# Optimization experiments

Hardware: AMD Instinct MI355X
Metric: run time of the kernel (lower is better)

Reference implementation:

```python
import jax, jax.numpy as jnp
import numpy as np

N = 50000          # nodes
DEG = 16           # out-degree
E = N * DEG        # edges
IN = 256           # input feature dim
H = 8              # hidden heads
DH = 32            # per-head hidden dim (hidden_dim // H)
HID = H * DH       # 256
OUT = 64           # output dim (single output head)
ALPHA = 0.2        # LeakyReLU negative slope


def _xavier(k, shape, fan_in, fan_out):
    limit = 1.414 * np.sqrt(6.0 / (fan_in + fan_out))
    return jax.random.uniform(k, shape, jnp.float32, -limit, limit)


def setup_inputs() -> dict:
    key = jax.random.key(0)
    ks = jax.random.split(key, 6)
    X = jax.random.normal(ks[0], (N, IN), jnp.float32)
    src = jnp.repeat(jnp.arange(N, dtype=jnp.int32), DEG)      # every row non-empty
    dst = jax.random.randint(ks[1], (E,), 0, N, jnp.int32)
    edges = jnp.stack([src, dst])                               # [2, E]
    W0 = _xavier(ks[2], (H, IN, DH), IN, DH)
    a0 = _xavier(ks[3], (H, 2 * DH), 2 * DH, 1)
    W1 = _xavier(ks[4], (1, HID, OUT), HID, OUT)
    a1 = _xavier(ks[5], (1, 2 * OUT), 2 * OUT, 1)
    return {"X": X, "edges": edges, "W0": W0, "a0": a0, "W1": W1, "a1": a1}


def sparse_gat_layer(X, edges, W, a):
    # W: [H, Din, D], a: [H, 2D]. Equivalent to concat(h_src, h_dst) @ a split.
    n = X.shape[0]
    D = W.shape[2]
    src, dst = edges[0], edges[1]
    h = jnp.einsum('nd,hde->hne', X, W)                         # [H, N, D]
    s_src = jnp.einsum('hne,he->hn', h, a[:, :D])               # [H, N]
    s_dst = jnp.einsum('hne,he->hn', h, a[:, D:])               # [H, N]
    e = jax.nn.leaky_relu(s_src[:, src] + s_dst[:, dst], ALPHA)  # [H, E]
    # stable per-row (segment = src) softmax, matching torch.sparse.softmax(dim=1)
    seg_max = jax.lax.stop_gradient(
        jax.vmap(lambda v: jax.ops.segment_max(v, src, num_segments=n))(e))
    p = jnp.exp(e - seg_max[:, src])
    denom = jax.vmap(lambda v: jax.ops.segment_sum(v, src, num_segments=n))(p)
    att = p / denom[:, src]                                      # [H, E]
    # out[i] = sum_{e: src=i} att_e * h[dst_e]
    agg = jax.vmap(lambda a_, hh: jax.ops.segment_sum(a_[:, None] * hh[dst], src,
                                                      num_segments=n))(att, h)
    return agg                                                   # [H, N, D]


def reference(X, edges, W0, a0, W1, a1):
    h1 = jax.nn.elu(sparse_gat_layer(X, edges, W0, a0))          # [H, N, DH]
    X1 = jnp.transpose(h1, (1, 0, 2)).reshape(X.shape[0], -1)    # concat heads [N, HID]
    out = sparse_gat_layer(X1, edges, W1, a1)                    # [1, N, OUT]
    return jax.nn.elu(out[0])                                    # num_heads_out = 1
```

## Files before the change

### kernel.cpp

```cpp
#include <hip/hip_runtime.h>

typedef __attribute__((ext_vector_type(8))) short bh8;
typedef __attribute__((ext_vector_type(4))) float f4;

static __device__ __forceinline__ float b2f(unsigned short u){
  union { unsigned int i; float f; } c; c.i = ((unsigned int)u) << 16; return c.f;
}
static __device__ __forceinline__ unsigned short f2b(float f){
  union { float f; unsigned int i; } c; c.f = f;
  unsigned int u = c.i; u += 0x7fffu + ((u >> 16) & 1u);
  return (unsigned short)(u >> 16);
}
static __device__ __forceinline__ float elu1(float x){ return x > 0.f ? x : (__expf(x) - 1.f); }
static __device__ __forceinline__ float lrelu(float x){ return x > 0.f ? x : 0.2f * x; }
static __device__ __forceinline__ float gload(const void* p, size_t i, int isf32){
  return isf32 ? ((const float*)p)[i] : b2f(((const unsigned short*)p)[i]);
}
static __device__ __forceinline__ int detect_f32(const unsigned int* __restrict__ W0w, int lane){
  unsigned int w = W0w[lane & 63];
  unsigned int e = (w >> 7) & 0xFFu;
  unsigned long long m = __ballot(e >= 100u && e <= 126u);
  return (__popcll(m) < 32) ? 1 : 0;
}

__global__ __launch_bounds__(256) void prep_kernel(
    const void* __restrict__ W0, const void* __restrict__ a0,
    const void* __restrict__ W1, const void* __restrict__ a1,
    unsigned short* __restrict__ Wt1, unsigned short* __restrict__ Wt2){
  int isf = detect_f32((const unsigned int*)W0, threadIdx.x & 63);
  int c = blockIdx.x, k = threadIdx.x;
  if (c < 272){
    float v;
    if (c < 256){
      int h = c >> 5, d = c & 31;
      v = gload(W0, (size_t)(h*256 + k)*32 + d, isf);
    } else if (c < 264){
      int h = c - 256; float s = 0.f;
      for (int d = 0; d < 32; d++)
        s += gload(W0, (size_t)(h*256 + k)*32 + d, isf) * gload(a0, h*64 + d, isf);
      v = s;
    } else {
      int h = c - 264; float s = 0.f;
      for (int d = 0; d < 32; d++)
        s += gload(W0, (size_t)(h*256 + k)*32 + d, isf) * gload(a0, h*64 + 32 + d, isf);
      v = s;
    }
    Wt1[c*256 + k] = f2b(v);
  } else {
    int c2 = c - 272; float v;
    if (c2 < 64) v = gload(W1, k*64 + c2, isf);
    else if (c2 == 64){ float s = 0.f; for (int i = 0; i < 64; i++) s += gload(W1, k*64+i, isf) * gload(a1, i, isf);      v = s; }
    else if (c2 == 65){ float s = 0.f; for (int i = 0; i < 64; i++) s += gload(W1, k*64+i, isf) * gload(a1, 64 + i, isf); v = s; }
    else v = 0.f;
    Wt2[c2*256 + k] = f2b(v);
  }
}

__global__ __launch_bounds__(256, 2) void gemm1_mfma(
    const void* __restrict__ Xraw, const unsigned short* __restrict__ Wt,
    unsigned short* __restrict__ H1, float* __restrict__ S1, int N,
    const void* __restrict__ W0){
  __shared__ __align__(16) unsigned short A[112*264];
  int tid = threadIdx.x, wv = tid >> 6, lane = tid & 63;
  int isf = detect_f32((const unsigned int*)W0, lane);
  int q = lane >> 4, l = lane & 15;
  int n0 = blockIdx.x*112;
  #pragma unroll
  for (int it = 0; it < 14; it++){
    int g = it*256 + tid;
    int r = g >> 5, c = g & 31;
    int grow = n0 + r; if (grow > N-1) grow = N-1;
    bh8 v;
    if (isf){
      const float* xr = (const float*)Xraw + (size_t)grow*256 + c*8;
      float4 u0 = *(const float4*)xr, u1 = *(const float4*)(xr + 4);
      v[0]=(short)f2b(u0.x); v[1]=(short)f2b(u0.y); v[2]=(short)f2b(u0.z); v[3]=(short)f2b(u0.w);
      v[4]=(short)f2b(u1.x); v[5]=(short)f2b(u1.y); v[6]=(short)f2b(u1.z); v[7]=(short)f2b(u1.w);
    } else {
      v = *(const bh8*)((const unsigned short*)Xraw + (size_t)grow*256 + c*8);
    }
    *(bh8*)&A[r*264 + c*8] = v;
  }
  __syncthreads();
  const bh8* Wb = (const bh8*)Wt;
  bh8 B[4][8];
  #pragma unroll
  for (int tt = 0; tt < 4; tt++){
    int t = wv*4 + tt;
    #pragma unroll
    for (int kk = 0; kk < 8; kk++) B[tt][kk] = Wb[(size_t)(t*16 + l)*32 + kk*4 + q];
  }
  bh8 Bs[8];
  if (wv == 0){
    #pragma unroll
    for (int kk = 0; kk < 8; kk++) Bs[kk] = Wb[(size_t)(256 + l)*32 + kk*4 + q];
  }
  for (int m = 0; m < 7; m++){
    bh8 a[8];
    #pragma unroll
    for (int kk = 0; kk < 8; kk++) a[kk] = *(const bh8*)&A[(m*16 + l)*264 + kk*32 + q*8];
    f4 acc[4];
    #pragma unroll
    for (int tt = 0; tt < 4; tt++){
      f4 z = {0.f,0.f,0.f,0.f}; acc[tt] = z;
      #pragma unroll
      for (int kk = 0; kk < 8; kk++)
        acc[tt] = __builtin_amdgcn_mfma_f32_16x16x32_bf16(a[kk], B[tt][kk], acc[tt], 0, 0, 0);
    }
    if (wv == 0){
      f4 as = {0.f,0.f,0.f,0.f};
      #pragma unroll
      for (int kk = 0; kk < 8; kk++)
        as = __builtin_amdgcn_mfma_f32_16x16x32_bf16(a[kk], Bs[kk], as, 0, 0, 0);
      #pragma unroll
      for (int r = 0; r < 4; r++){
        int row = n0 + m*16 + q*4 + r;
        if (row < N) S1[(size_t)row*16 + l] = as[r];
      }
    }
    __syncthreads();
    #pragma unroll
    for (int tt = 0; tt < 4; tt++){
      int t = wv*4 + tt;
      #pragma unroll
      for (int r = 0; r < 4; r++)
        A[(m*16 + q*4 + r)*264 + t*16 + l] = f2b(acc[tt][r]);
    }
    __syncthreads();
  }
  #pragma unroll
  for (int g = 0; g < 14; g++){
    int idx = g*256 + tid;
    int r = idx >> 5, c = idx & 31;
    int row = n0 + r;
    if (row < N)
      *(bh8*)(H1 + (size_t)row*256 + c*8) = *(const bh8*)&A[r*264 + c*8];
  }
}

__global__ __launch_bounds__(256) void fused_agg1_gemm2(
    const float* __restrict__ S1, const unsigned short* __restrict__ H1,
    const int* __restrict__ dst, const unsigned short* __restrict__ Wt2,
    unsigned short* __restrict__ H2, float* __restrict__ S2, int N){
  __shared__ __align__(16) unsigned short Xt[16*264];
  __shared__ __align__(16) unsigned short Hs[16*88];
  int tid = threadIdx.x, wv = tid >> 6, lane = tid & 63;
  int n0 = blockIdx.x*16;
  int h = lane >> 3, jj = lane & 7;
  int half = lane >> 5, li = lane & 31;
  int cb = li*8, hc = li >> 2;
  for (int np = 0; np < 2; np++){
    int lrA = wv*4 + np*2, lrB = lrA + 1;
    int nodeA = n0 + lrA; if (nodeA > N-1) nodeA = N-1;
    int nodeB = n0 + lrB; if (nodeB > N-1) nodeB = N-1;
    const int* dpA = dst + (size_t)nodeA*16;
    const int* dpB = dst + (size_t)nodeB*16;
    int d0A = dpA[jj], d1A = dpA[jj + 8];
    int d0B = dpB[jj], d1B = dpB[jj + 8];
    float ssA = S1[(size_t)nodeA*16 + h];
    float ssB = S1[(size_t)nodeB*16 + h];
    float e0A = lrelu(ssA + S1[(size_t)d0A*16 + 8 + h]);
    float e1A = lrelu(ssA + S1[(size_t)d1A*16 + 8 + h]);
    float e0B = lrelu(ssB + S1[(size_t)d0B*16 + 8 + h]);
    float e1B = lrelu(ssB + S1[(size_t)d1B*16 + 8 + h]);
    float mA = fmaxf(e0A, e1A), mB = fmaxf(e0B, e1B);
    mA = fmaxf(mA, __shfl_xor(mA, 1)); mB = fmaxf(mB, __shfl_xor(mB, 1));
    mA = fmaxf(mA, __shfl_xor(mA, 2)); mB = fmaxf(mB, __shfl_xor(mB, 2));
    mA = fmaxf(mA, __shfl_xor(mA, 4)); mB = fmaxf(mB, __shfl_xor(mB, 4));
    float p0A = __expf(e0A - mA), p1A = __expf(e1A - mA);
    float p0B = __expf(e0B - mB), p1B = __expf(e1B - mB);
    float sA = p0A + p1A, sB = p0B + p1B;
    sA += __shfl_xor(sA, 1); sB += __shfl_xor(sB, 1);
    sA += __shfl_xor(sA, 2); sB += __shfl_xor(sB, 2);
    sA += __shfl_xor(sA, 4); sB += __shfl_xor(sB, 4);
    float invA = 1.f / sA, invB = 1.f / sB;
    float v0A = p0A * invA, v1A = p1A * invA;
    float v0B = p0B * invB, v1B = p1B * invB;
    float accA[8] = {0.f,0.f,0.f,0.f,0.f,0.f,0.f,0.f};
    float accB[8] = {0.f,0.f,0.f,0.f,0.f,0.f,0.f,0.f};
    #pragma unroll
    for (int i = 0; i < 8; i++){
      int j  = i*2 + half;
      int jl = j & 7;
      int rowA  = (i < 4) ? __shfl(d0A, jl) : __shfl(d1A, jl);
      int rowB  = (i < 4) ? __shfl(d0B, jl) : __shfl(d1B, jl);
      float awA = (i < 4) ? __shfl(v0A, hc*8 + jl) : __shfl(v1A, hc*8 + jl);
      float awB = (i < 4) ? __shfl(v0B, hc*8 + jl) : __shfl(v1B, hc*8 + jl);
      bh8 vA = *(const bh8*)(H1 + (size_t)rowA*256 + cb);
      bh8 vB = *(const bh8*)(H1 + (size_t)rowB*256 + cb);
      #pragma unroll
      for (int c = 0; c < 8; c++){
        accA[c] += awA * b2f((unsigned short)vA[c]);
        accB[c] += awB * b2f((unsigned short)vB[c]);
      }
    }
    #pragma unroll
    for (int c = 0; c < 8; c++){
      accA[c] += __shfl_xor(accA[c], 32);
      accB[c] += __shfl_xor(accB[c], 32);
    }
    if (half == 0){
      bh8 oA, oB;
      #pragma unroll
      for (int c = 0; c < 8; c++){
        oA[c] = (short)f2b(elu1(accA[c]));
        oB[c] = (short)f2b(elu1(accB[c]));
      }
      *(bh8*)&Xt[lrA*264 + cb] = oA;
      *(bh8*)&Xt[lrB*264 + cb] = oB;
    }
  }
  __syncthreads();
  {
    int q = lane >> 4, l = lane & 15;
    bh8 a[8];
    #pragma unroll
    for (int kk = 0; kk < 8; kk++)
      a[kk] = *(const bh8*)&Xt[l*264 + kk*32 + q*8];
    const bh8* Wb = (const bh8*)Wt2;
    int ntt = (wv == 3) ? 2 : 1;
    for (int it = 0; it < ntt; it++){
      int tt = (it == 0) ? wv : 4;
      bh8 b[8];
      #pragma unroll
      for (int kk = 0; kk < 8; kk++) b[kk] = Wb[(size_t)(tt*16 + l)*32 + kk*4 + q];
      f4 c0 = {0.f,0.f,0.f,0.f};
      #pragma unroll
      for (int kk = 0; kk < 8; kk++)
        c0 = __builtin_amdgcn_mfma_f32_16x16x32_bf16(a[kk], b[kk], c0, 0, 0, 0);
      if (tt < 4){
        #pragma unroll
        for (int r = 0; r < 4; r++)
          Hs[(q*4 + r)*88 + tt*16 + l] = f2b(c0[r]);
      } else if (l < 2){
        #pragma unroll
        for (int r = 0; r < 4; r++){
          int row0 = n0 + q*4 + r;
          if (row0 < N) S2[(size_t)row0*2 + l] = c0[r];
        }
      }
    }
  }
  __syncthreads();
  if (tid < 128){
    int r2 = tid >> 3, ch = tid & 7;
    int row = n0 + r2;
    if (row < N)
      *(bh8*)(H2 + (size_t)row*64 + ch*8) = *(const bh8*)&Hs[r2*88 + ch*8];
  }
}

__global__ __launch_bounds__(256) void agg2_kernel(
    const float* __restrict__ S2, const unsigned short* __restrict__ H2,
    const int* __restrict__ dst, void* __restrict__ outv, int N,
    const void* __restrict__ W0){
  int tid = threadIdx.x, wv = tid >> 6, lane = tid & 63;
  int isf = detect_f32((const unsigned int*)W0, lane);
  int nodeA = blockIdx.x*8 + wv*2; if (nodeA > N-1) nodeA = N-1;
  int nodeB = nodeA + 1;           if (nodeB > N-1) nodeB = N-1;
  int j = lane & 15;
  int dA = dst[(size_t)nodeA*16 + j];
  int dB = dst[(size_t)nodeB*16 + j];
  float eA = lrelu(S2[(size_t)nodeA*2] + S2[(size_t)dA*2 + 1]);
  float eB = lrelu(S2[(size_t)nodeB*2] + S2[(size_t)dB*2 + 1]);
  float mA = eA, mB = eB;
  mA = fmaxf(mA, __shfl_xor(mA, 1)); mB = fmaxf(mB, __shfl_xor(mB, 1));
  mA = fmaxf(mA, __shfl_xor(mA, 2)); mB = fmaxf(mB, __shfl_xor(mB, 2));
  mA = fmaxf(mA, __shfl_xor(mA, 4)); mB = fmaxf(mB, __shfl_xor(mB, 4));
  mA = fmaxf(mA, __shfl_xor(mA, 8)); mB = fmaxf(mB, __shfl_xor(mB, 8));
  float pA = __expf(eA - mA), pB = __expf(eB - mB);
  float sA = pA, sB = pB;
  sA += __shfl_xor(sA, 1); sB += __shfl_xor(sB, 1);
  sA += __shfl_xor(sA, 2); sB += __shfl_xor(sB, 2);
  sA += __shfl_xor(sA, 4); sB += __shfl_xor(sB, 4);
  sA += __shfl_xor(sA, 8); sB += __shfl_xor(sB, 8);
  float attA = pA / sA, attB = pB / sB;
  int g = lane >> 3, cbl = (lane & 7)*8;
  float accA[8] = {0.f,0.f,0.f,0.f,0.f,0.f,0.f,0.f};
  float accB[8] = {0.f,0.f,0.f,0.f,0.f,0.f,0.f,0.f};
  #pragma unroll
  for (int it = 0; it < 2; it++){
    int j2 = it*8 + g;
    float awA = __shfl(attA, j2), awB = __shfl(attB, j2);
    int rowA  = __shfl(dA,   j2), rowB  = __shfl(dB,   j2);
    bh8 vA = *(const bh8*)(H2 + (size_t)rowA*64 + cbl);
    bh8 vB = *(const bh8*)(H2 + (size_t)rowB*64 + cbl);
    #pragma unroll
    for (int c = 0; c < 8; c++){
      accA[c] += awA * b2f((unsigned short)vA[c]);
      accB[c] += awB * b2f((unsigned short)vB[c]);
    }
  }
  #pragma unroll
  for (int c = 0; c < 8; c++){
    accA[c] += __shfl_xor(accA[c], 8);  accB[c] += __shfl_xor(accB[c], 8);
    accA[c] += __shfl_xor(accA[c], 16); accB[c] += __shfl_xor(accB[c], 16);
    accA[c] += __shfl_xor(accA[c], 32); accB[c] += __shfl_xor(accB[c], 32);
  }
  if (lane < 8){
    size_t oiA = (size_t)nodeA*64 + cbl;
    size_t oiB = (size_t)nodeB*64 + cbl;
    if (isf){
      float4 a0v, a1v, b0v, b1v;
      a0v.x = elu1(accA[0]); a0v.y = elu1(accA[1]); a0v.z = elu1(accA[2]); a0v.w = elu1(accA[3]);
      a1v.x = elu1(accA[4]); a1v.y = elu1(accA[5]); a1v.z = elu1(accA[6]); a1v.w = elu1(accA[7]);
      b0v.x = elu1(accB[0]); b0v.y = elu1(accB[1]); b0v.z = elu1(accB[2]); b0v.w = elu1(accB[3]);
      b1v.x = elu1(accB[4]); b1v.y = elu1(accB[5]); b1v.z = elu1(accB[6]); b1v.w = elu1(accB[7]);
      *(float4*)((float*)outv + oiA)     = a0v;
      *(float4*)((float*)outv + oiA + 4) = a1v;
      *(float4*)((float*)outv + oiB)     = b0v;
      *(float4*)((float*)outv + oiB + 4) = b1v;
    } else {
      bh8 oA, oB;
      #pragma unroll
      for (int c = 0; c < 8; c++){
        oA[c] = (short)f2b(elu1(accA[c]));
        oB[c] = (short)f2b(elu1(accB[c]));
      }
      *(bh8*)((unsigned short*)outv + oiA) = oA;
      *(bh8*)((unsigned short*)outv + oiB) = oB;
    }
  }
}

extern "C" void kernel_launch(void* const* d_in, const int* in_sizes, int n_in,
                              void* d_out, int out_size, void* d_ws, size_t ws_size,
                              hipStream_t stream){
  const void* X  = d_in[0];
  const int*  ed = (const int*)d_in[1];
  const void* W0 = d_in[2];
  const void* a0 = d_in[3];
  const void* W1 = d_in[4];
  const void* a1 = d_in[5];

  int N = in_sizes[0] / 256;
  int E = N * 16;
  const int* dst = ed + E;

  char* w = (char*)d_ws;
  size_t off = 0;
  auto alloc = [&](size_t bytes) -> void* {
    void* p = w + off; off += (bytes + 255) & ~(size_t)255; return p;
  };
  unsigned short* Wt1 = (unsigned short*)alloc(272*256*2);
  unsigned short* Wt2 = (unsigned short*)alloc(80*256*2);
  float*          S1  = (float*)alloc((size_t)N*16*4);
  unsigned short* H1  = (unsigned short*)alloc((size_t)N*256*2);
  unsigned short* H2  = (unsigned short*)alloc((size_t)N*64*2);
  float*          S2  = (float*)alloc((size_t)N*2*4);
  (void)ws_size; (void)n_in; (void)out_size;

  int g1 = (N + 111) / 112;
  int gf = (N + 15) / 16;
  int ab = (N + 7) / 8;
  prep_kernel     <<<352,256, 0, stream>>>(W0, a0, W1, a1, Wt1, Wt2);
  gemm1_mfma      <<<g1, 256, 0, stream>>>(X,  Wt1, H1, S1, N, W0);
  fused_agg1_gemm2<<<gf, 256, 0, stream>>>(S1, H1, dst, Wt2, H2, S2, N);
  agg2_kernel     <<<ab, 256, 0, stream>>>(S2, H2, dst, d_out, N, W0);
}
```

Measured before the change: 214.7 us.

## Restructure gemm1 to kk-outer loop with per-wave output staging and smaller tiles

The first GEMM kernel now uses 80-row tiles instead of 112, raising the occupancy hint to 3 blocks per SM. The loop order becomes K-outer: B fragments are loaded one kk at a time from global memory and reused across five row tiles with all accumulators held in registers. This removes the per-m-tile __syncthreads pairs, and the epilogue stages results in a small per-wave LDS scratch buffer before writing H1 directly. It trades higher accumulator register pressure and more B reloads per block for fewer barriers and less shared memory.

```diff
diff --git a/kernel.cpp b/kernel.cpp
--- a/kernel.cpp
+++ b/kernel.cpp
@@ -56,17 +56,17 @@
   }
 }
 
-__global__ __launch_bounds__(256, 2) void gemm1_mfma(
+__global__ __launch_bounds__(256, 3) void gemm1_mfma(
     const void* __restrict__ Xraw, const unsigned short* __restrict__ Wt,
     unsigned short* __restrict__ H1, float* __restrict__ S1, int N,
     const void* __restrict__ W0){
-  __shared__ __align__(16) unsigned short A[112*264];
+  __shared__ __align__(16) unsigned short A[80*264];
   int tid = threadIdx.x, wv = tid >> 6, lane = tid & 63;
   int isf = detect_f32((const unsigned int*)W0, lane);
   int q = lane >> 4, l = lane & 15;
-  int n0 = blockIdx.x*112;
-  #pragma unroll
-  for (int it = 0; it < 14; it++){
+  int n0 = blockIdx.x*80;
+  #pragma unroll
+  for (int it = 0; it < 10; it++){
     int g = it*256 + tid;
     int r = g >> 5, c = g & 31;
     int grow = n0 + r; if (grow > N-1) grow = N-1;
@@ -83,58 +83,57 @@
   }
   __syncthreads();
   const bh8* Wb = (const bh8*)Wt;
-  bh8 B[4][8];
-  #pragma unroll
-  for (int tt = 0; tt < 4; tt++){
-    int t = wv*4 + tt;
-    #pragma unroll
-    for (int kk = 0; kk < 8; kk++) B[tt][kk] = Wb[(size_t)(t*16 + l)*32 + kk*4 + q];
-  }
-  bh8 Bs[8];
-  if (wv == 0){
-    #pragma unroll
-    for (int kk = 0; kk < 8; kk++) Bs[kk] = Wb[(size_t)(256 + l)*32 + kk*4 + q];
-  }
-  for (int m = 0; m < 7; m++){
-    bh8 a[8];
-    #pragma unroll
-    for (int kk = 0; kk < 8; kk++) a[kk] = *(const bh8*)&A[(m*16 + l)*264 + kk*32 + q*8];
-    f4 acc[4];
-    #pragma unroll
-    for (int tt = 0; tt < 4; tt++){
-      f4 z = {0.f,0.f,0.f,0.f}; acc[tt] = z;
-      #pragma unroll
-      for (int kk = 0; kk < 8; kk++)
-        acc[tt] = __builtin_amdgcn_mfma_f32_16x16x32_bf16(a[kk], B[tt][kk], acc[tt], 0, 0, 0);
-    }
+  f4 acc[5][4];
+  f4 accS[5];
+  f4 z = {0.f,0.f,0.f,0.f};
+  #pragma unroll
+  for (int m = 0; m < 5; m++){
+    accS[m] = z;
+    #pragma unroll
+    for (int tt = 0; tt < 4; tt++) acc[m][tt] = z;
+  }
+  #pragma unroll
+  for (int kk = 0; kk < 8; kk++){
+    bh8 B0 = Wb[(size_t)((wv*4+0)*16 + l)*32 + kk*4 + q];
+    bh8 B1 = Wb[(size_t)((wv*4+1)*16 + l)*32 + kk*4 + q];
+    bh8 B2 = Wb[(size_t)((wv*4+2)*16 + l)*32 + kk*4 + q];
+    bh8 B3 = Wb[(size_t)((wv*4+3)*16 + l)*32 + kk*4 + q];
+    bh8 Bs;
+    if (wv == 0) Bs = Wb[(size_t)(256 + l)*32 + kk*4 + q];
+    #pragma unroll
+    for (int m = 0; m < 5; m++){
+      bh8 a = *(const bh8*)&A[(m*16 + l)*264 + kk*32 + q*8];
+      acc[m][0] = __builtin_amdgcn_mfma_f32_16x16x32_bf16(a, B0, acc[m][0], 0, 0, 0);
+      acc[m][1] = __builtin_amdgcn_mfma_f32_16x16x32_bf16(a, B1, acc[m][1], 0, 0, 0);
+      acc[m][2] = __builtin_amdgcn_mfma_f32_16x16x32_bf16(a, B2, acc[m][2], 0, 0, 0);
+      acc[m][3] = __builtin_amdgcn_mfma_f32_16x16x32_bf16(a, B3, acc[m][3], 0, 0, 0);
+      if (wv == 0)
+        accS[m] = __builtin_amdgcn_mfma_f32_16x16x32_bf16(a, Bs, accS[m], 0, 0, 0);
+    }
+  }
+  __syncthreads();
+  unsigned short* cs = &A[wv*1152];
+  #pragma unroll
+  for (int m = 0; m < 5; m++){
+    #pragma unroll
+    for (int tt = 0; tt < 4; tt++)
+      #pragma unroll
+      for (int r = 0; r < 4; r++)
+        cs[(q*4 + r)*72 + tt*16 + l] = f2b(acc[m][tt][r]);
     if (wv == 0){
-      f4 as = {0.f,0.f,0.f,0.f};
-      #pragma unroll
-      for (int kk = 0; kk < 8; kk++)
-        as = __builtin_amdgcn_mfma_f32_16x16x32_bf16(a[kk], Bs[kk], as, 0, 0, 0);
       #pragma unroll
       for (int r = 0; r < 4; r++){
         int row = n0 + m*16 + q*4 + r;
-        if (row < N) S1[(size_t)row*16 + l] = as[r];
-      }
-    }
-    __syncthreads();
-    #pragma unroll
-    for (int tt = 0; tt < 4; tt++){
-      int t = wv*4 + tt;
-      #pragma unroll
-      for (int r = 0; r < 4; r++)
-        A[(m*16 + q*4 + r)*264 + t*16 + l] = f2b(acc[tt][r]);
-    }
-    __syncthreads();
-  }
-  #pragma unroll
-  for (int g = 0; g < 14; g++){
-    int idx = g*256 + tid;
-    int r = idx >> 5, c = idx & 31;
-    int row = n0 + r;
-    if (row < N)
-      *(bh8*)(H1 + (size_t)row*256 + c*8) = *(const bh8*)&A[r*264 + c*8];
+        if (row < N) S1[(size_t)row*16 + l] = accS[m][r];
+      }
+    }
+    #pragma unroll
+    for (int it2 = 0; it2 < 2; it2++){
+      int r2 = lane & 15, ch = (lane >> 4) + it2*4;
+      int row = n0 + m*16 + r2;
+      if (row < N)
+        *(bh8*)(H1 + (size_t)row*256 + wv*64 + ch*8) = *(const bh8*)&cs[r2*72 + ch*8];
+    }
   }
 }
 
@@ -350,7 +349,7 @@
   float*          S2  = (float*)alloc((size_t)N*2*4);
   (void)ws_size; (void)n_in; (void)out_size;
 
-  int g1 = (N + 111) / 112;
+  int g1 = (N + 79) / 80;
   int gf = (N + 15) / 16;
   int ab = (N + 7) / 8;
   prep_kernel     <<<352,256, 0, stream>>>(W0, a0, W1, a1, Wt1, Wt2);
```

Measured after the change: 212.5 us. Within noise of the previous version (-1.0%).
